# Kernel optimization log

Measured on AMD Instinct MI355X. Metric: run time of the kernel, lower is better.

The kernel has to match this reference:

```python
import jax, jax.numpy as jnp
import numpy as np

N, E, G = 10000, 320000, 256
IN, H, FP, OUT = 128, 256, 5000, 138


def setup_inputs() -> dict:
    key = jax.random.key(0)
    ks = jax.random.split(key, 12)
    x = jax.random.normal(ks[0], (N, IN), dtype=jnp.float32)
    edge_index = jax.random.randint(ks[1], (2, E), 0, N, dtype=jnp.int64)
    batch_index = jnp.sort(jax.random.randint(ks[2], (N,), 0, G, dtype=jnp.int64))
    grover_fp = jax.random.normal(ks[3], (G, FP), dtype=jnp.float32)
    def lin(k, fan_in, fan_out):
        lim = 1.0 / np.sqrt(fan_in)
        return jax.random.uniform(k, (fan_in, fan_out), jnp.float32, -lim, lim)
    W1 = lin(ks[4], IN, H);            b1 = jnp.zeros((H,), jnp.float32)
    W2 = lin(ks[5], H, H);             b2 = jnp.zeros((H,), jnp.float32)
    Wm1 = lin(ks[6], H + FP, H);       bm1 = jnp.zeros((H,), jnp.float32)
    Wm2 = lin(ks[7], H, OUT);          bm2 = jnp.zeros((OUT,), jnp.float32)
    return {"x": x, "edge_index": edge_index, "batch_index": batch_index,
            "grover_fp": grover_fp, "W1": W1, "b1": b1, "W2": W2, "b2": b2,
            "Wm1": Wm1, "bm1": bm1, "Wm2": Wm2, "bm2": bm2}


def reference(x, edge_index, batch_index, grover_fp, W1, b1, W2, b2, Wm1, bm1, Wm2, bm2):
    n = x.shape[0]
    # GCNConv: add self-loops, symmetric degree normalization D^-1/2 (A+I) D^-1/2
    loop = jnp.arange(n, dtype=edge_index.dtype)
    src = jnp.concatenate([edge_index[0], loop])  # [E+N]
    dst = jnp.concatenate([edge_index[1], loop])
    deg = jax.ops.segment_sum(jnp.ones_like(src, dtype=x.dtype), dst, num_segments=n)
    dinv = jax.lax.rsqrt(jnp.maximum(deg, 1.0))
    norm = dinv[src] * dinv[dst]  # [E+N]

    def gcn(h, W, b):
        hw = h @ W                              # [N, H]
        msg = hw[src] * norm[:, None]           # gather + normalize
        return jax.ops.segment_sum(msg, dst, num_segments=n) + b  # scatter-add

    h = jax.nn.relu(gcn(x, W1, b1))
    h = jax.nn.relu(gcn(h, W2, b2))

    # global mean pool over graphs
    sums = jax.ops.segment_sum(h, batch_index, num_segments=G)        # [G, H]
    cnts = jax.ops.segment_sum(jnp.ones((n,), h.dtype), batch_index, num_segments=G)
    gnn_repr = sums / jnp.maximum(cnts, 1.0)[:, None]

    hcat = jnp.concatenate([gnn_repr, grover_fp], axis=-1)  # [G, H+FP]
    # MLP (dropout is identity in eval mode)
    return jax.nn.relu(hcat @ Wm1 + bm1) @ Wm2 + bm2        # [G, OUT]
```

## Files before the change

### kernel.cpp

```cpp
#include <hip/hip_runtime.h>

constexpr int N_NODES = 10000;
constexpr int E_EDGES = 320000;
constexpr int G_GRAPHS = 256;
constexpr int IN_F = 128;
constexpr int H_F = 256;
constexpr int FP_F = 5000;
constexpr int OUT_F = 138;
constexpr int KCAT = H_F + FP_F;
constexpr int KPAD = 5376;
constexpr int KZ = 21;
constexpr int DMAX = 128;

constexpr int ZB = (N_NODES + 255) / 256;
constexpr int PREP_TOT = H_F * IN_F + H_F * H_F + G_GRAPHS * (KPAD - H_F);
constexpr int PB = (PREP_TOT + 255) / 256;
constexpr int HB = (E_EDGES + 255) / 256;
constexpr int WT_TILES = (KPAD / 64) * (H_F / 64);
constexpr int GB = 157 * 4;
constexpr int M1B = (KZ - 1) * 16;

typedef __attribute__((ext_vector_type(8))) short short8;
typedef __attribute__((ext_vector_type(4))) float f32x4;

static __device__ __forceinline__ unsigned short f2bf(float f) {
    union { float f; unsigned u; } a; a.f = f;
    unsigned r = a.u + 0x7fffu + ((a.u >> 16) & 1u);
    return (unsigned short)(r >> 16);
}
static __device__ __forceinline__ float bf2f(unsigned short u) {
    union { unsigned u; float f; } a; a.u = ((unsigned)u) << 16;
    return a.f;
}

template <int K, bool AF32>
__device__ __forceinline__ void gemm_tile(unsigned short* a_lds, unsigned short* w_lds,
                                          const void* __restrict__ Asrc,
                                          const unsigned short* __restrict__ Wt,
                                          unsigned short* __restrict__ C,
                                          int bm0, int bn0, int tid) {
    constexpr int KB = 128;
    const int lane = tid & 63;
    const int wv = tid >> 6;

    f32x4 acc[4] = {};
    const int rA = wv * 16 + (lane & 15);
    const int kq = (lane >> 4) * 8;

    for (int kb = 0; kb < K; kb += KB) {
        for (int c = tid; c < 64 * KB / 8; c += 256) {
            int r = c >> 4;
            int k = (c & 15) * 8;
            int gr = bm0 + r;
            short8 v = {};
            if (gr < N_NODES) {
                if (AF32) {
                    const float* A = (const float*)Asrc;
                    const float* p = A + (size_t)gr * K + kb + k;
                    float4 lo = *reinterpret_cast<const float4*>(p);
                    float4 hi = *reinterpret_cast<const float4*>(p + 4);
                    v[0] = (short)f2bf(lo.x); v[1] = (short)f2bf(lo.y);
                    v[2] = (short)f2bf(lo.z); v[3] = (short)f2bf(lo.w);
                    v[4] = (short)f2bf(hi.x); v[5] = (short)f2bf(hi.y);
                    v[6] = (short)f2bf(hi.z); v[7] = (short)f2bf(hi.w);
                } else {
                    const unsigned short* A = (const unsigned short*)Asrc;
                    v = *reinterpret_cast<const short8*>(A + (size_t)gr * K + kb + k);
                }
            }
            int byte = r * (2 * KB) + ((2 * k) ^ ((r & 7) << 4));
            *reinterpret_cast<short8*>((char*)a_lds + byte) = v;
        }
        for (int c = tid; c < 64 * KB / 8; c += 256) {
            int r = c >> 4;
            int k = (c & 15) * 8;
            short8 v = *reinterpret_cast<const short8*>(Wt + (size_t)(bn0 + r) * K + kb + k);
            int byte = r * (2 * KB) + ((2 * k) ^ ((r & 7) << 4));
            *reinterpret_cast<short8*>((char*)w_lds + byte) = v;
        }
        __syncthreads();
#pragma unroll
        for (int t = 0; t < KB / 32; ++t) {
            const int k0 = t * 32 + kq;
            short8 af = *reinterpret_cast<const short8*>(
                (char*)a_lds + rA * (2 * KB) + ((2 * k0) ^ ((rA & 7) << 4)));
#pragma unroll
            for (int nt = 0; nt < 4; ++nt) {
                const int rW = nt * 16 + (lane & 15);
                short8 bfr = *reinterpret_cast<const short8*>(
                    (char*)w_lds + rW * (2 * KB) + ((2 * k0) ^ ((rW & 7) << 4)));
                acc[nt] = __builtin_amdgcn_mfma_f32_16x16x32_bf16(bfr, af, acc[nt], 0, 0, 0);
            }
        }
        __syncthreads();
    }

    const int row = bm0 + wv * 16 + (lane & 15);
    if (row < N_NODES) {
#pragma unroll
        for (int nt = 0; nt < 4; ++nt) {
            int col = bn0 + nt * 16 + (lane >> 4) * 4;
            ushort4 o;
            o.x = f2bf(acc[nt][0]);
            o.y = f2bf(acc[nt][1]);
            o.z = f2bf(acc[nt][2]);
            o.w = f2bf(acc[nt][3]);
            *reinterpret_cast<ushort4*>(C + (size_t)row * H_F + col) = o;
        }
    }
}

__device__ __forceinline__ void mlp1_tile(unsigned short* a_lds, unsigned short* w_lds,
                                          const unsigned short* __restrict__ hcat,
                                          const unsigned short* __restrict__ Wt,
                                          float* __restrict__ pz,
                                          int bm0, int bn0, int kz0, int tid) {
    constexpr int KB = 128;
    const int lane = tid & 63;
    const int wv = tid >> 6;

    f32x4 acc[4] = {};
    const int rA = wv * 16 + (lane & 15);
    const int kq = (lane >> 4) * 8;

    for (int kb = kz0; kb < kz0 + 256; kb += KB) {
        for (int c = tid; c < 64 * KB / 8; c += 256) {
            int r = c >> 4;
            int k = (c & 15) * 8;
            short8 v = *reinterpret_cast<const short8*>(hcat + (size_t)(bm0 + r) * KPAD + kb + k);
            int byte = r * (2 * KB) + ((2 * k) ^ ((r & 7) << 4));
            *reinterpret_cast<short8*>((char*)a_lds + byte) = v;
        }
        for (int c = tid; c < 64 * KB / 8; c += 256) {
            int r = c >> 4;
            int k = (c & 15) * 8;
            short8 v = *reinterpret_cast<const short8*>(Wt + (size_t)(bn0 + r) * KPAD + kb + k);
            int byte = r * (2 * KB) + ((2 * k) ^ ((r & 7) << 4));
            *reinterpret_cast<short8*>((char*)w_lds + byte) = v;
        }
        __syncthreads();
#pragma unroll
        for (int t = 0; t < KB / 32; ++t) {
            const int k0 = t * 32 + kq;
            short8 af = *reinterpret_cast<const short8*>(
                (char*)a_lds + rA * (2 * KB) + ((2 * k0) ^ ((rA & 7) << 4)));
#pragma unroll
            for (int nt = 0; nt < 4; ++nt) {
                const int rW = nt * 16 + (lane & 15);
                short8 bfr = *reinterpret_cast<const short8*>(
                    (char*)w_lds + rW * (2 * KB) + ((2 * k0) ^ ((rW & 7) << 4)));
                acc[nt] = __builtin_amdgcn_mfma_f32_16x16x32_bf16(bfr, af, acc[nt], 0, 0, 0);
            }
        }
        __syncthreads();
    }

    const int row = bm0 + wv * 16 + (lane & 15);
#pragma unroll
    for (int nt = 0; nt < 4; ++nt) {
        int col = bn0 + nt * 16 + (lane >> 4) * 4;
        float4 o; o.x = acc[nt][0]; o.y = acc[nt][1]; o.z = acc[nt][2]; o.w = acc[nt][3];
        *reinterpret_cast<float4*>(pz + (size_t)row * H_F + col) = o;
    }
}

__global__ void k_p1(const float* __restrict__ W1, const float* __restrict__ W2,
                     const float* __restrict__ gfp, int* __restrict__ cnt,
                     unsigned short* __restrict__ W1t, unsigned short* __restrict__ W2t,
                     unsigned short* __restrict__ hcat) {
    const int bx = blockIdx.x;
    if (bx < ZB) {
        int i = bx * 256 + threadIdx.x;
        if (i < N_NODES) cnt[i] = 0;
        return;
    }
    int i = (bx - ZB) * 256 + threadIdx.x;
    if (i < H_F * IN_F) {
        int c = i / IN_F, k = i - c * IN_F;
        W1t[i] = f2bf(W1[(size_t)k * H_F + c]);
        return;
    }
    i -= H_F * IN_F;
    if (i < H_F * H_F) {
        int c = i >> 8, k = i & 255;
        W2t[i] = f2bf(W2[(size_t)k * H_F + c]);
        return;
    }
    i -= H_F * H_F;
    const int W = KPAD - H_F;
    if (i < G_GRAPHS * W) {
        int g = i / W, k = i - g * W;
        hcat[(size_t)g * KPAD + H_F + k] = (k < FP_F) ? f2bf(gfp[(size_t)g * FP_F + k])
                                                      : (unsigned short)0;
    }
}

__global__ void k_p2(const int* __restrict__ ei, int* __restrict__ cnt,
                     int* __restrict__ srcs_pad,
                     const float* __restrict__ Wm1, unsigned short* __restrict__ Wt) {
    const int bx = blockIdx.x;
    if (bx < HB) {
        int e = bx * 256 + threadIdx.x;
        if (e < E_EDGES) {
            int s = ei[e];
            int d = ei[E_EDGES + e];
            int p = atomicAdd(&cnt[d], 1);
            if (p < DMAX) srcs_pad[(d << 7) + p] = s;
        }
        return;
    }
    __shared__ float tbuf[64][65];
    const int tile = bx - HB;
    const int k0 = (tile % (KPAD / 64)) * 64;
    const int c0 = (tile / (KPAD / 64)) * 64;
    for (int idx = threadIdx.x; idx < 64 * 64; idx += 256) {
        int r = idx >> 6, cc = idx & 63;
        int k = k0 + r;
        tbuf[r][cc] = (k < KCAT) ? Wm1[(size_t)k * H_F + c0 + cc] : 0.0f;
    }
    __syncthreads();
    for (int idx = threadIdx.x; idx < 64 * 64; idx += 256) {
        int r = idx >> 6, kk = idx & 63;
        Wt[(size_t)(c0 + r) * KPAD + k0 + kk] = f2bf(tbuf[kk][r]);
    }
}

__global__ __launch_bounds__(256) void k_p3(const float* __restrict__ x,
                                            const unsigned short* __restrict__ W1t,
                                            unsigned short* __restrict__ Abf,
                                            const int* __restrict__ cnt,
                                            float* __restrict__ dinv) {
    __shared__ unsigned short a_lds[64 * 128];
    __shared__ unsigned short w_lds[64 * 128];
    const int bx = blockIdx.x;
    if (bx < GB) {
        gemm_tile<IN_F, true>(a_lds, w_lds, x, W1t, Abf, (bx % 157) * 64, (bx / 157) * 64,
                              threadIdx.x);
        return;
    }
    int i = (bx - GB) * 256 + threadIdx.x;
    if (i < N_NODES) dinv[i] = rsqrtf((float)cnt[i] + 1.0f);
}

__global__ __launch_bounds__(256) void k_agg(const unsigned short* __restrict__ hw,
                                             const int* __restrict__ cnt,
                                             const int* __restrict__ srcs_pad,
                                             const float* __restrict__ dinv,
                                             const float* __restrict__ b,
                                             unsigned short* __restrict__ outp) {
    const int lane = threadIdx.x & 63;
    const int node = __builtin_amdgcn_readfirstlane(blockIdx.x * 4 + (threadIdx.x >> 6));
    const float dd = dinv[node];
    const unsigned short* rowb = hw + lane * 4;
    const int* sp = srcs_pad + (node << 7);

    float a0, a1, a2, a3;
    {
        const ushort4 sv = *reinterpret_cast<const ushort4*>(hw + (size_t)node * H_F + lane * 4);
        const float4 bv = *reinterpret_cast<const float4*>(b + lane * 4);
        const float ddsq = dd * dd;
        a0 = bf2f(sv.x) * ddsq + bv.x;
        a1 = bf2f(sv.y) * ddsq + bv.y;
        a2 = bf2f(sv.z) * ddsq + bv.z;
        a3 = bf2f(sv.w) * ddsq + bv.w;
    }

    const int e1 = __builtin_amdgcn_readfirstlane(min(cnt[node], DMAX));
    int e = 0;
    for (; e + 8 <= e1; e += 8) {
        ushort4 v[8];
        float w[8];
#pragma unroll
        for (int q = 0; q < 8; ++q) {
            const int s = sp[e + q];
            w[q] = dinv[s] * dd;
            v[q] = *reinterpret_cast<const ushort4*>(rowb + (size_t)s * H_F);
        }
#pragma unroll
        for (int q = 0; q < 8; ++q) {
            a0 += bf2f(v[q].x) * w[q];
            a1 += bf2f(v[q].y) * w[q];
            a2 += bf2f(v[q].z) * w[q];
            a3 += bf2f(v[q].w) * w[q];
        }
    }
    for (; e < e1; ++e) {
        const int s = sp[e];
        const float w = dinv[s] * dd;
        const ushort4 v = *reinterpret_cast<const ushort4*>(rowb + (size_t)s * H_F);
        a0 += bf2f(v.x) * w;
        a1 += bf2f(v.y) * w;
        a2 += bf2f(v.z) * w;
        a3 += bf2f(v.w) * w;
    }
    ushort4 o;
    o.x = f2bf(fmaxf(a0, 0.0f));
    o.y = f2bf(fmaxf(a1, 0.0f));
    o.z = f2bf(fmaxf(a2, 0.0f));
    o.w = f2bf(fmaxf(a3, 0.0f));
    *reinterpret_cast<ushort4*>(outp + (size_t)node * H_F + lane * 4) = o;
}

__global__ __launch_bounds__(256) void k_p5(const unsigned short* __restrict__ h1,
                                            const unsigned short* __restrict__ W2t,
                                            unsigned short* __restrict__ Abf,
                                            const unsigned short* __restrict__ hcat,
                                            const unsigned short* __restrict__ Wm1t,
                                            float* __restrict__ partial) {
    __shared__ unsigned short a_lds[64 * 128];
    __shared__ unsigned short w_lds[64 * 128];
    int bx = blockIdx.x;
    if (bx < GB) {
        gemm_tile<H_F, false>(a_lds, w_lds, h1, W2t, Abf, (bx % 157) * 64, (bx / 157) * 64,
                              threadIdx.x);
        return;
    }
    bx -= GB;
    const int z = bx / 16 + 1;
    const int r = bx % 16;
    mlp1_tile(a_lds, w_lds, hcat, Wm1t, partial + (size_t)(z - 1) * (G_GRAPHS * H_F),
              (r & 3) * 64, (r >> 2) * 64, z * 256, threadIdx.x);
}

__global__ void k_fin(const unsigned short* __restrict__ h1, const int* __restrict__ batch,
                      const unsigned short* __restrict__ Wm1t,
                      const float* __restrict__ partial, const float* __restrict__ bm1,
                      const float* __restrict__ Wm2, const float* __restrict__ bm2,
                      float* __restrict__ out) {
    __shared__ float m[H_F];
    __shared__ float hrow[H_F];
    const int g = blockIdx.x;
    const int j = threadIdx.x;
    int lo = 0, hi = N_NODES;
    while (lo < hi) { int mm = (lo + hi) >> 1; if (batch[mm] < g) lo = mm + 1; else hi = mm; }
    const int s = lo;
    lo = s; hi = N_NODES;
    while (lo < hi) { int mm = (lo + hi) >> 1; if (batch[mm] < g + 1) lo = mm + 1; else hi = mm; }
    const int e = lo;
    float c0 = 0.0f, c1 = 0.0f, c2 = 0.0f, c3 = 0.0f;
    int i = s;
    for (; i + 4 <= e; i += 4) {
        c0 += bf2f(h1[(size_t)(i + 0) * H_F + j]);
        c1 += bf2f(h1[(size_t)(i + 1) * H_F + j]);
        c2 += bf2f(h1[(size_t)(i + 2) * H_F + j]);
        c3 += bf2f(h1[(size_t)(i + 3) * H_F + j]);
    }
    for (; i < e; ++i) c0 += bf2f(h1[(size_t)i * H_F + j]);
    hrow[j] = ((c0 + c1) + (c2 + c3)) / fmaxf((float)(e - s), 1.0f);
    __syncthreads();

    float acc = bm1[j];
    for (int k = 0; k < H_F; k += 8) {
        short8 wv = *reinterpret_cast<const short8*>(Wm1t + (size_t)j * KPAD + k);
#pragma unroll
        for (int q = 0; q < 8; ++q) acc += hrow[k + q] * bf2f((unsigned short)wv[q]);
    }
    for (int z = 0; z < KZ - 1; ++z)
        acc += partial[((size_t)z * G_GRAPHS + g) * H_F + j];
    m[j] = fmaxf(acc, 0.0f);
    __syncthreads();
    if (j < OUT_F) {
        float a = bm2[j];
        for (int k = 0; k < H_F; ++k) a += m[k] * Wm2[k * OUT_F + j];
        out[g * OUT_F + j] = a;
    }
}

extern "C" void kernel_launch(void* const* d_in, const int* in_sizes, int n_in,
                              void* d_out, int out_size, void* d_ws, size_t ws_size,
                              hipStream_t stream) {
    const float* x       = (const float*)d_in[0];
    const int*   ei      = (const int*)d_in[1];
    const int*   batch   = (const int*)d_in[2];
    const float* gfp     = (const float*)d_in[3];
    const float* W1      = (const float*)d_in[4];
    const float* b1      = (const float*)d_in[5];
    const float* W2      = (const float*)d_in[6];
    const float* b2      = (const float*)d_in[7];
    const float* Wm1     = (const float*)d_in[8];
    const float* bm1     = (const float*)d_in[9];
    const float* Wm2     = (const float*)d_in[10];
    const float* bm2     = (const float*)d_in[11];
    float* out = (float*)d_out;

    float* dinv = (float*)d_ws;
    unsigned short* W1t  = (unsigned short*)(dinv + N_NODES);
    unsigned short* W2t  = W1t + IN_F * H_F;
    unsigned short* Abf  = W2t + H_F * H_F;
    unsigned short* h1   = Abf + (size_t)N_NODES * H_F;
    unsigned short* hcat = h1 + (size_t)N_NODES * H_F;
    unsigned short* Wm1t = hcat + (size_t)G_GRAPHS * KPAD;
    float* partial = (float*)(Wm1t + (size_t)H_F * KPAD);
    int* cnt      = (int*)(partial + (size_t)(KZ - 1) * G_GRAPHS * H_F);
    int* srcs_pad = cnt + N_NODES;

    k_p1<<<ZB + PB, 256, 0, stream>>>(W1, W2, gfp, cnt, W1t, W2t, hcat);

    k_p2<<<HB + WT_TILES, 256, 0, stream>>>(ei, cnt, srcs_pad, Wm1, Wm1t);

    k_p3<<<GB + ZB, 256, 0, stream>>>(x, W1t, Abf, cnt, dinv);

    k_agg<<<N_NODES / 4, 256, 0, stream>>>(Abf, cnt, srcs_pad, dinv, b1, h1);

    k_p5<<<GB + M1B, 256, 0, stream>>>(h1, W2t, Abf, hcat, Wm1t, partial);

    k_agg<<<N_NODES / 4, 256, 0, stream>>>(Abf, cnt, srcs_pad, dinv, b2, h1);

    k_fin<<<G_GRAPHS, H_F, 0, stream>>>(h1, batch, Wm1t, partial, bm1, Wm2, bm2, out);
}
```

Baseline: 116.0 us.

## Regroup kernel stages and compute degree normalization inline instead of storing dinv

```diff
diff --git a/kernel.cpp b/kernel.cpp
--- a/kernel.cpp
+++ b/kernel.cpp
@@ -19,6 +19,7 @@
 constexpr int WT_TILES = (KPAD / 64) * (H_F / 64);
 constexpr int GB = 157 * 4;
 constexpr int M1B = (KZ - 1) * 16;
+constexpr int AB = N_NODES / 4;
 
 typedef __attribute__((ext_vector_type(8))) short short8;
 typedef __attribute__((ext_vector_type(4))) float f32x4;
@@ -164,93 +165,15 @@
     }
 }
 
-__global__ void k_p1(const float* __restrict__ W1, const float* __restrict__ W2,
-                     const float* __restrict__ gfp, int* __restrict__ cnt,
-                     unsigned short* __restrict__ W1t, unsigned short* __restrict__ W2t,
-                     unsigned short* __restrict__ hcat) {
-    const int bx = blockIdx.x;
-    if (bx < ZB) {
-        int i = bx * 256 + threadIdx.x;
-        if (i < N_NODES) cnt[i] = 0;
-        return;
-    }
-    int i = (bx - ZB) * 256 + threadIdx.x;
-    if (i < H_F * IN_F) {
-        int c = i / IN_F, k = i - c * IN_F;
-        W1t[i] = f2bf(W1[(size_t)k * H_F + c]);
-        return;
-    }
-    i -= H_F * IN_F;
-    if (i < H_F * H_F) {
-        int c = i >> 8, k = i & 255;
-        W2t[i] = f2bf(W2[(size_t)k * H_F + c]);
-        return;
-    }
-    i -= H_F * H_F;
-    const int W = KPAD - H_F;
-    if (i < G_GRAPHS * W) {
-        int g = i / W, k = i - g * W;
-        hcat[(size_t)g * KPAD + H_F + k] = (k < FP_F) ? f2bf(gfp[(size_t)g * FP_F + k])
-                                                      : (unsigned short)0;
-    }
-}
-
-__global__ void k_p2(const int* __restrict__ ei, int* __restrict__ cnt,
-                     int* __restrict__ srcs_pad,
-                     const float* __restrict__ Wm1, unsigned short* __restrict__ Wt) {
-    const int bx = blockIdx.x;
-    if (bx < HB) {
-        int e = bx * 256 + threadIdx.x;
-        if (e < E_EDGES) {
-            int s = ei[e];
-            int d = ei[E_EDGES + e];
-            int p = atomicAdd(&cnt[d], 1);
-            if (p < DMAX) srcs_pad[(d << 7) + p] = s;
-        }
-        return;
-    }
-    __shared__ float tbuf[64][65];
-    const int tile = bx - HB;
-    const int k0 = (tile % (KPAD / 64)) * 64;
-    const int c0 = (tile / (KPAD / 64)) * 64;
-    for (int idx = threadIdx.x; idx < 64 * 64; idx += 256) {
-        int r = idx >> 6, cc = idx & 63;
-        int k = k0 + r;
-        tbuf[r][cc] = (k < KCAT) ? Wm1[(size_t)k * H_F + c0 + cc] : 0.0f;
-    }
-    __syncthreads();
-    for (int idx = threadIdx.x; idx < 64 * 64; idx += 256) {
-        int r = idx >> 6, kk = idx & 63;
-        Wt[(size_t)(c0 + r) * KPAD + k0 + kk] = f2bf(tbuf[kk][r]);
-    }
-}
-
-__global__ __launch_bounds__(256) void k_p3(const float* __restrict__ x,
-                                            const unsigned short* __restrict__ W1t,
-                                            unsigned short* __restrict__ Abf,
-                                            const int* __restrict__ cnt,
-                                            float* __restrict__ dinv) {
-    __shared__ unsigned short a_lds[64 * 128];
-    __shared__ unsigned short w_lds[64 * 128];
-    const int bx = blockIdx.x;
-    if (bx < GB) {
-        gemm_tile<IN_F, true>(a_lds, w_lds, x, W1t, Abf, (bx % 157) * 64, (bx / 157) * 64,
-                              threadIdx.x);
-        return;
-    }
-    int i = (bx - GB) * 256 + threadIdx.x;
-    if (i < N_NODES) dinv[i] = rsqrtf((float)cnt[i] + 1.0f);
-}
-
-__global__ __launch_bounds__(256) void k_agg(const unsigned short* __restrict__ hw,
-                                             const int* __restrict__ cnt,
-                                             const int* __restrict__ srcs_pad,
-                                             const float* __restrict__ dinv,
-                                             const float* __restrict__ b,
-                                             unsigned short* __restrict__ outp) {
-    const int lane = threadIdx.x & 63;
-    const int node = __builtin_amdgcn_readfirstlane(blockIdx.x * 4 + (threadIdx.x >> 6));
-    const float dd = dinv[node];
+__device__ __forceinline__ void agg_body(const unsigned short* __restrict__ hw,
+                                         const int* __restrict__ cnt,
+                                         const int* __restrict__ srcs_pad,
+                                         const float* __restrict__ b,
+                                         unsigned short* __restrict__ outp,
+                                         int node_base, int tid) {
+    const int lane = tid & 63;
+    const int node = __builtin_amdgcn_readfirstlane(node_base + (tid >> 6));
+    const float dd = rsqrtf((float)cnt[node] + 1.0f);
     const unsigned short* rowb = hw + lane * 4;
     const int* sp = srcs_pad + (node << 7);
 
@@ -273,7 +196,7 @@
 #pragma unroll
         for (int q = 0; q < 8; ++q) {
             const int s = sp[e + q];
-            w[q] = dinv[s] * dd;
+            w[q] = rsqrtf((float)cnt[s] + 1.0f) * dd;
             v[q] = *reinterpret_cast<const ushort4*>(rowb + (size_t)s * H_F);
         }
 #pragma unroll
@@ -286,7 +209,7 @@
     }
     for (; e < e1; ++e) {
         const int s = sp[e];
-        const float w = dinv[s] * dd;
+        const float w = rsqrtf((float)cnt[s] + 1.0f) * dd;
         const ushort4 v = *reinterpret_cast<const ushort4*>(rowb + (size_t)s * H_F);
         a0 += bf2f(v.x) * w;
         a1 += bf2f(v.y) * w;
@@ -301,25 +224,117 @@
     *reinterpret_cast<ushort4*>(outp + (size_t)node * H_F + lane * 4) = o;
 }
 
-__global__ __launch_bounds__(256) void k_p5(const unsigned short* __restrict__ h1,
-                                            const unsigned short* __restrict__ W2t,
+__global__ void k_p1(const float* __restrict__ W1, const float* __restrict__ W2,
+                     const float* __restrict__ gfp, int* __restrict__ cnt,
+                     unsigned short* __restrict__ W1t, unsigned short* __restrict__ W2t,
+                     unsigned short* __restrict__ hcat) {
+    const int bx = blockIdx.x;
+    if (bx < ZB) {
+        int i = bx * 256 + threadIdx.x;
+        if (i < N_NODES) cnt[i] = 0;
+        return;
+    }
+    int i = (bx - ZB) * 256 + threadIdx.x;
+    if (i < H_F * IN_F) {
+        int c = i / IN_F, k = i - c * IN_F;
+        W1t[i] = f2bf(W1[(size_t)k * H_F + c]);
+        return;
+    }
+    i -= H_F * IN_F;
+    if (i < H_F * H_F) {
+        int c = i >> 8, k = i & 255;
+        W2t[i] = f2bf(W2[(size_t)k * H_F + c]);
+        return;
+    }
+    i -= H_F * H_F;
+    const int W = KPAD - H_F;
+    if (i < G_GRAPHS * W) {
+        int g = i / W, k = i - g * W;
+        hcat[(size_t)g * KPAD + H_F + k] = (k < FP_F) ? f2bf(gfp[(size_t)g * FP_F + k])
+                                                      : (unsigned short)0;
+    }
+}
+
+__global__ __launch_bounds__(256) void k_p2(const float* __restrict__ x,
+                                            const unsigned short* __restrict__ W1t,
                                             unsigned short* __restrict__ Abf,
+                                            const int* __restrict__ ei,
+                                            int* __restrict__ cnt,
+                                            int* __restrict__ srcs_pad,
+                                            const float* __restrict__ Wm1,
+                                            unsigned short* __restrict__ Wt) {
+    __shared__ unsigned short a_lds[64 * 128];
+    __shared__ unsigned short w_lds[64 * 128];
+    int bx = blockIdx.x;
+    if (bx < GB) {
+        gemm_tile<IN_F, true>(a_lds, w_lds, x, W1t, Abf, (bx % 157) * 64, (bx / 157) * 64,
+                              threadIdx.x);
+        return;
+    }
+    bx -= GB;
+    if (bx < HB) {
+        int e = bx * 256 + threadIdx.x;
+        if (e < E_EDGES) {
+            int s = ei[e];
+            int d = ei[E_EDGES + e];
+            int p = atomicAdd(&cnt[d], 1);
+            if (p < DMAX) srcs_pad[(d << 7) + p] = s;
+        }
+        return;
+    }
+    bx -= HB;
+    float* tbuf = (float*)a_lds;
+    const int k0 = (bx % (KPAD / 64)) * 64;
+    const int c0 = (bx / (KPAD / 64)) * 64;
+    for (int idx = threadIdx.x; idx < 64 * 64; idx += 256) {
+        int r = idx >> 6, cc = idx & 63;
+        int k = k0 + r;
+        tbuf[r * 65 + cc] = (k < KCAT) ? Wm1[(size_t)k * H_F + c0 + cc] : 0.0f;
+    }
+    __syncthreads();
+    for (int idx = threadIdx.x; idx < 64 * 64; idx += 256) {
+        int r = idx >> 6, kk = idx & 63;
+        Wt[(size_t)(c0 + r) * KPAD + k0 + kk] = f2bf(tbuf[kk * 65 + r]);
+    }
+}
+
+__global__ __launch_bounds__(256) void k_p3(const unsigned short* __restrict__ Abf,
+                                            const int* __restrict__ cnt,
+                                            const int* __restrict__ srcs_pad,
+                                            const float* __restrict__ b1,
+                                            unsigned short* __restrict__ h1,
                                             const unsigned short* __restrict__ hcat,
                                             const unsigned short* __restrict__ Wm1t,
                                             float* __restrict__ partial) {
     __shared__ unsigned short a_lds[64 * 128];
     __shared__ unsigned short w_lds[64 * 128];
     int bx = blockIdx.x;
-    if (bx < GB) {
-        gemm_tile<H_F, false>(a_lds, w_lds, h1, W2t, Abf, (bx % 157) * 64, (bx / 157) * 64,
-                              threadIdx.x);
-        return;
-    }
-    bx -= GB;
+    if (bx < AB) {
+        agg_body(Abf, cnt, srcs_pad, b1, h1, bx * 4, threadIdx.x);
+        return;
+    }
+    bx -= AB;
     const int z = bx / 16 + 1;
     const int r = bx % 16;
     mlp1_tile(a_lds, w_lds, hcat, Wm1t, partial + (size_t)(z - 1) * (G_GRAPHS * H_F),
               (r & 3) * 64, (r >> 2) * 64, z * 256, threadIdx.x);
+}
+
+__global__ __launch_bounds__(256) void k_p4(const unsigned short* __restrict__ h1,
+                                            const unsigned short* __restrict__ W2t,
+                                            unsigned short* __restrict__ Abf) {
+    __shared__ unsigned short a_lds[64 * 128];
+    __shared__ unsigned short w_lds[64 * 128];
+    gemm_tile<H_F, false>(a_lds, w_lds, h1, W2t, Abf, (blockIdx.x % 157) * 64,
+                          (blockIdx.x / 157) * 64, threadIdx.x);
+}
+
+__global__ __launch_bounds__(256) void k_p5(const unsigned short* __restrict__ Abf,
+                                            const int* __restrict__ cnt,
+                                            const int* __restrict__ srcs_pad,
+                                            const float* __restrict__ b2,
+                                            unsigned short* __restrict__ h1) {
+    agg_body(Abf, cnt, srcs_pad, b2, h1, blockIdx.x * 4, threadIdx.x);
 }
 
 __global__ void k_fin(const unsigned short* __restrict__ h1, const int* __restrict__ batch,
@@ -383,8 +398,7 @@
     const float* bm2     = (const float*)d_in[11];
     float* out = (float*)d_out;
 
-    float* dinv = (float*)d_ws;
-    unsigned short* W1t  = (unsigned short*)(dinv + N_NODES);
+    unsigned short* W1t  = (unsigned short*)d_ws;
     unsigned short* W2t  = W1t + IN_F * H_F;
     unsigned short* Abf  = W2t + H_F * H_F;
     unsigned short* h1   = Abf + (size_t)N_NODES * H_F;
@@ -396,15 +410,16 @@
 
     k_p1<<<ZB + PB, 256, 0, stream>>>(W1, W2, gfp, cnt, W1t, W2t, hcat);
 
-    k_p2<<<HB + WT_TILES, 256, 0, stream>>>(ei, cnt, srcs_pad, Wm1, Wm1t);
-
-    k_p3<<<GB + ZB, 256, 0, stream>>>(x, W1t, Abf, cnt, dinv);
-
-    k_agg<<<N_NODES / 4, 256, 0, stream>>>(Abf, cnt, srcs_pad, dinv, b1, h1);
-
-    k_p5<<<GB + M1B, 256, 0, stream>>>(h1, W2t, Abf, hcat, Wm1t, partial);
-
-    k_agg<<<N_NODES / 4, 256, 0, stream>>>(Abf, cnt, srcs_pad, dinv, b2, h1);
+    k_p2<<<GB + HB + WT_TILES, 256, 0, stream>>>(x, W1t, Abf, ei, cnt, srcs_pad, Wm1, Wm1t);
+
+    k_p3<<<AB + M1B, 256, 0, stream>>>(Abf, cnt, srcs_pad, b1, h1, hcat, Wm1t, partial);
+
+    {
+        dim3 g2(157 * 4);
+        k_p4<<<g2, 256, 0, stream>>>(h1, W2t, Abf);
+    }
+
+    k_p5<<<AB, 256, 0, stream>>>(Abf, cnt, srcs_pad, b2, h1);
 
     k_fin<<<G_GRAPHS, H_F, 0, stream>>>(h1, batch, Wm1t, partial, bm1, Wm2, bm2, out);
 }
```

After: 112.5 us. 1.03x faster.
